# Kernel optimization log

Measured on AMD Instinct MI355X. Metric: run time of the kernel, lower is better.

The kernel has to match this reference:

```python
import jax, jax.numpy as jnp
import numpy as np
import math

B, D, NH, NS, NT = 16, 256, 512, 8, 32
NV = NS * NT          # 256 prediction variables
L, H, A = 4, 8, 64    # attention layers, heads, head dim
HA = H * A            # 512
M = 512               # mlp_dim
R = 128               # resolution
EPS = 1e-5


def setup_inputs() -> dict:
    key = jax.random.key(0)
    ks = jax.random.split(key, 32)
    s = 0.02
    inp = {
        'hist_encoded': jax.random.normal(ks[0], (B, NH, D), jnp.float32),
        'hist_true_u': jax.random.uniform(ks[1], (B, NH), jnp.float32),
        'pred_encoded': jax.random.normal(ks[2], (B, NV, D), jnp.float32),
        'pred_true_u': jax.random.uniform(ks[3], (B, NV), jnp.float32),
        # dimension shifting layer
        'ds_w': jax.random.normal(ks[4], (D, HA), jnp.float32) * s,
        'ds_b': jnp.zeros((HA,), jnp.float32),
        # per-layer, per-head key/value creators: Linear(D+1 -> A)
        'key_w': jax.random.normal(ks[5], (L, H, D + 1, A), jnp.float32) * s,
        'key_b': jnp.zeros((L, H, A), jnp.float32),
        'val_w': jax.random.normal(ks[6], (L, H, D + 1, A), jnp.float32) * s,
        'val_b': jnp.zeros((L, H, A), jnp.float32),
        # layer norms
        'ln1_g': jnp.ones((L, HA), jnp.float32),
        'ln1_b': jnp.zeros((L, HA), jnp.float32),
        'ln2_g': jnp.ones((L, HA), jnp.float32),
        'ln2_b': jnp.zeros((L, HA), jnp.float32),
        # feed-forward (mlp_layers=2): HA->M, M->M, M->HA
        'ff_w1': jax.random.normal(ks[7], (L, HA, M), jnp.float32) * s,
        'ff_b1': jnp.zeros((L, M), jnp.float32),
        'ff_w2': jax.random.normal(ks[8], (L, M, M), jnp.float32) * s,
        'ff_b2': jnp.zeros((L, M), jnp.float32),
        'ff_w3': jax.random.normal(ks[9], (L, M, HA), jnp.float32) * s,
        'ff_b3': jnp.zeros((L, HA), jnp.float32),
        # dist extractor
        'de_w': jax.random.normal(ks[10], (HA, R), jnp.float32) * s,
        'de_b': jnp.zeros((R,), jnp.float32),
        'num_series': NS,
        'num_timesteps': NT,
    }
    return inp


def _ln(x, g, b):
    m = x.mean(-1, keepdims=True)
    v = ((x - m) ** 2).mean(-1, keepdims=True)
    return g * (x - m) / jnp.sqrt(v + EPS) + b


def _forward(hist_encoded, hist_true_u, pred_encoded, pred_true_u,
             ds_w, ds_b, key_w, key_b, val_w, val_b,
             ln1_g, ln1_b, ln2_g, ln2_b,
             ff_w1, ff_b1, ff_w2, ff_b2, ff_w3, ff_b3,
             de_w, de_b):
    Bm, NVm, Dm = pred_encoded.shape
    NHm = hist_encoded.shape[1]
    Lm, Hm, _, Am = key_w.shape
    W = NHm + NVm
    # identity permutation in the source loss() -> no-op
    att = pred_encoded @ ds_w + ds_b  # [B, NV, HA]
    # key/value inputs: [hist||u ; pred||u] -> [B, W, D+1]
    ki = jnp.concatenate([
        jnp.concatenate([hist_encoded, hist_true_u[:, :, None]], axis=2),
        jnp.concatenate([pred_encoded, pred_true_u[:, :, None]], axis=2)], axis=1)
    keys = jnp.einsum('bwd,lhda->lbhwa', ki, key_w) + key_b[:, None, :, None, :]
    vals = jnp.einsum('bwd,lhda->lbhwa', ki, val_w) + val_b[:, None, :, None, :]
    # flipped-triangular mask: position w is masked iff w >= NH + v
    mask = jnp.arange(W)[None, :] >= (NHm + jnp.arange(NVm)[:, None])  # [NV, W]
    scale = Am ** (-0.5)
    for l in range(Lm):
        avh = att.reshape(Bm, NVm, Hm, Am)
        prod = jnp.einsum('bvhi,bhwi->bhvw', avh, keys[l])  # [B,H,NV,W]
        prod = jnp.where(mask, -jnp.inf, prod) * scale
        w = jax.nn.softmax(prod, axis=-1)
        a = jnp.einsum('bhvw,bhwj->bvhj', w, vals[l]).reshape(Bm, NVm, Hm * Am)
        att = _ln(att + a, ln1_g[l], ln1_b[l])
        ff = jnp.maximum(att @ ff_w1[l] + ff_b1[l], 0.0)
        ff = jnp.maximum(ff @ ff_w2[l] + ff_b2[l], 0.0)
        ff = ff @ ff_w3[l] + ff_b3[l]
        att = _ln(att + ff, ln2_g[l], ln2_b[l])
    res = de_w.shape[-1]
    target = jnp.clip(jnp.floor(pred_true_u[:, 1:] * res).astype(jnp.int32), 0, res - 1)
    logits = (att @ de_w + de_b)[:, 1:, :]
    lp = math.log(res) + jax.nn.log_softmax(logits, axis=2)
    lp = jnp.take_along_axis(lp, target[:, :, None], axis=2)[:, :, 0]
    return -lp.sum(axis=1)  # [B]


def reference(hist_encoded, hist_true_u, pred_encoded, pred_true_u,
              ds_w, ds_b, key_w, key_b, val_w, val_b,
              ln1_g, ln1_b, ln2_g, ln2_b,
              ff_w1, ff_b1, ff_w2, ff_b2, ff_w3, ff_b3,
              de_w, de_b, num_series, num_timesteps):
    assert pred_encoded.shape[1] == num_series * num_timesteps
    return _forward(hist_encoded, hist_true_u, pred_encoded, pred_true_u,
                    ds_w, ds_b, key_w, key_b, val_w, val_b,
                    ln1_g, ln1_b, ln2_g, ln2_b,
                    ff_w1, ff_b1, ff_w2, ff_b2, ff_w3, ff_b3,
                    de_w, de_b)
```

## Files before the change

### kernel.cpp

```cpp
#include <hip/hip_runtime.h>

constexpr int kB = 16, kD = 256, kNH = 512, kNV = 256, kW = 768;
constexpr int kL = 4, kH = 8, kA = 64, kHA = 512, kM = 512, kR = 128;
constexpr int kKP = 288;
constexpr int kRows = kB * kNV;

typedef __bf16 bf16x8 __attribute__((ext_vector_type(8)));
typedef __bf16 bf16x4 __attribute__((ext_vector_type(4)));
typedef float f32x4 __attribute__((ext_vector_type(4)));

__device__ inline void load_lds16(const __bf16* g, __bf16* l) {
  __builtin_amdgcn_global_load_lds(
      (const __attribute__((address_space(1))) void*)g,
      (__attribute__((address_space(3))) void*)l, 16, 0, 0);
}

constexpr int kP1 = kB * kW * kKP;
constexpr int kP2 = 4096 * kKP;
constexpr int kP3 = 12 * 512 * 512;
constexpr int kP4 = 200704;
constexpr int kP5 = 16;
constexpr int kPT = kP1 + kP2 + kP3 + kP4 + kP5;

__global__ void prep_kernel(const float* __restrict__ hist,
                            const float* __restrict__ hist_u,
                            const float* __restrict__ pred,
                            const float* __restrict__ pred_u,
                            const float* __restrict__ kw,
                            const float* __restrict__ vw,
                            const float* __restrict__ w1,
                            const float* __restrict__ w2,
                            const float* __restrict__ w3,
                            const float* __restrict__ ds_w,
                            const float* __restrict__ de_w,
                            const float* __restrict__ key_b,
                            const float* __restrict__ val_b,
                            __bf16* __restrict__ ki,
                            __bf16* __restrict__ kvwt,
                            __bf16* __restrict__ ffwt,
                            __bf16* __restrict__ ds_wt,
                            __bf16* __restrict__ de_wt,
                            float* __restrict__ kvb,
                            float* __restrict__ outz) {
  int i = blockIdx.x * 256 + threadIdx.x;
  if (i < kP1) {
    int d = i % kKP;
    int bw = i / kKP;
    int w = bw % kW;
    int b = bw / kW;
    float v = 0.f;
    if (d < 257) {
      if (w < kNH)
        v = (d < kD) ? hist[((size_t)b * kNH + w) * kD + d] : hist_u[b * kNH + w];
      else {
        int p = w - kNH;
        v = (d < kD) ? pred[((size_t)b * kNV + p) * kD + d] : pred_u[b * kNV + p];
      }
    }
    ki[i] = (__bf16)v;
  } else if (i < kP1 + kP2) {
    int j = i - kP1;
    int d = j % kKP;
    int c = j / kKP;
    float v = 0.f;
    if (d < 257) {
      bool isv = c >= 2048;
      int cc = isv ? c - 2048 : c;
      int l = cc >> 9, rest = cc & 511;
      int h = rest >> 6, a = rest & 63;
      size_t src = (((size_t)l * kH + h) * 257 + d) * kA + a;
      v = isv ? vw[src] : kw[src];
    }
    kvwt[j] = (__bf16)v;
  } else if (i < kP1 + kP2 + kP3) {
    int j = i - kP1 - kP2;
    int k = j & 511;
    int n = (j >> 9) & 511;
    int mat = j >> 18;
    int l = mat / 3, which = mat % 3;
    const float* src = which == 0 ? w1 : which == 1 ? w2 : w3;
    ffwt[j] = (__bf16)src[((size_t)l * 512 + k) * 512 + n];
  } else if (i < kP1 + kP2 + kP3 + kP4) {
    int j = i - kP1 - kP2 - kP3;
    if (j < 131072) {
      int n = j >> 8, k = j & 255;
      ds_wt[j] = (__bf16)ds_w[k * 512 + n];
    } else if (j < 196608) {
      int jj = j - 131072;
      int n = jj >> 9, k = jj & 511;
      de_wt[jj] = (__bf16)de_w[k * 128 + n];
    } else {
      int c = j - 196608;
      bool isv = c >= 2048;
      int cc = isv ? c - 2048 : c;
      int l = cc >> 9, rest = cc & 511;
      kvb[c] = isv ? val_b[l * 512 + rest] : key_b[l * 512 + rest];
    }
  } else if (i < kPT) {
    outz[i - kP1 - kP2 - kP3 - kP4] = 0.f;
  }
}

template <int BN, int OMODE, bool RELU, bool KIMAP, bool BIASROW>
__device__ __forceinline__ void gemm_core(
    int bxv, int byv, const __bf16* __restrict__ A,
    const __bf16* __restrict__ Bt, const float* __restrict__ bias,
    void* __restrict__ Cout, __bf16* __restrict__ Cout2, int K, int lda,
    int ldc, __bf16* As, __bf16* Bs) {
  constexpr int JN = BN / 32;
  constexpr int BROWS = BN / 4;
  const int t = threadIdx.x;
  const int wid = t >> 6;
  const int lane = t & 63;
  const int bm = byv * 128;
  const int bn = bxv * BN;
  const int wm = (wid >> 1) * 64;
  const int wn = (wid & 1) * (BN / 2);
  const int sr = lane >> 2, sc = lane & 3;
  const int skey = (sr >> 1) & 3;
  const int abase = KIMAP ? ((bm >> 8) * 768 + 512 + (bm & 255)) : bm;
  const __bf16* Ag = A + (size_t)(abase + wid * 32 + sr) * lda + (sc ^ skey) * 8;
  const __bf16* Bg = Bt + (size_t)(bn + wid * BROWS + sr) * K + (sc ^ skey) * 8;
  __bf16* AsW = As + (wid * 32) * 32;
  __bf16* BsW = Bs + (wid * BROWS) * 32;

  f32x4 acc[4][JN] = {};
  const int q = lane >> 4, mr = lane & 15;
  const int rkey = (mr >> 1) & 3;
  for (int k0 = 0; k0 < K; k0 += 32) {
    if (k0) __syncthreads();
    load_lds16(Ag + k0, AsW);
    load_lds16(Ag + (size_t)16 * lda + k0, AsW + 16 * 32);
    load_lds16(Bg + k0, BsW);
    if (BN == 128) load_lds16(Bg + (size_t)16 * K + k0, BsW + 16 * 32);
    __syncthreads();
    bf16x8 af[4], bfr[JN];
#pragma unroll
    for (int i = 0; i < 4; ++i)
      af[i] = *(const bf16x8*)(As + (wm + i * 16 + mr) * 32 + (q ^ rkey) * 8);
#pragma unroll
    for (int j = 0; j < JN; ++j)
      bfr[j] = *(const bf16x8*)(Bs + (wn + j * 16 + mr) * 32 + (q ^ rkey) * 8);
#pragma unroll
    for (int i = 0; i < 4; ++i)
#pragma unroll
      for (int j = 0; j < JN; ++j)
        acc[i][j] = __builtin_amdgcn_mfma_f32_16x16x32_bf16(af[i], bfr[j],
                                                            acc[i][j], 0, 0, 0);
  }
#pragma unroll
  for (int j = 0; j < JN; ++j) {
    int col = bn + wn + j * 16 + mr;
    float bscol = BIASROW ? 0.f : bias[col];
#pragma unroll
    for (int i = 0; i < 4; ++i) {
      int row0 = bm + wm + i * 16 + q * 4;
#pragma unroll
      for (int r = 0; r < 4; ++r) {
        float v = acc[i][j][r] + (BIASROW ? bias[row0 + r] : bscol);
        if (RELU) v = fmaxf(v, 0.f);
        size_t idx = (size_t)(row0 + r) * ldc + col;
        if (OMODE == 0) {
          ((float*)Cout)[idx] = v;
        } else if (OMODE == 1) {
          ((__bf16*)Cout)[idx] = (__bf16)v;
        } else {
          ((float*)Cout)[idx] = v;
          Cout2[idx] = (__bf16)v;
        }
      }
    }
  }
}

__global__ __launch_bounds__(256) void gemm3_kernel(
    const __bf16* __restrict__ ki, const __bf16* __restrict__ ds_wt,
    const float* __restrict__ ds_b, float* __restrict__ att,
    __bf16* __restrict__ att_bf, const __bf16* __restrict__ kv_wt,
    const float* __restrict__ kvb, __bf16* __restrict__ kvs_k,
    __bf16* __restrict__ vT) {
  __shared__ __align__(16) __bf16 smem[8192];
  __bf16* As = smem;
  __bf16* Bs = smem + 4096;
  int bid = blockIdx.x;
  if (bid < 256) {
    gemm_core<64, 2, false, true, false>(bid & 7, bid >> 3, ki, ds_wt, ds_b,
                                         att, att_bf, 256, kKP, 512, As, Bs);
  } else if (bid < 1792) {
    int b2 = bid - 256;
    gemm_core<128, 1, false, false, false>(b2 & 15, b2 >> 4, ki, kv_wt, kvb,
                                           kvs_k, nullptr, kKP, kKP, 2048, As,
                                           Bs);
  } else {
    int b3 = bid - 1792;
    gemm_core<128, 1, false, false, true>(b3 % 96, b3 / 96,
                                          kv_wt + (size_t)2048 * kKP, ki,
                                          kvb + 2048, vT, nullptr, kKP, kKP,
                                          12288, As, Bs);
  }
}

__global__ __launch_bounds__(256) void attn_kernel(
    const __bf16* __restrict__ attbf, const __bf16* __restrict__ kvs_k,
    const __bf16* __restrict__ vT, __bf16* __restrict__ outbf, int l) {
  const int u = blockIdx.x;
  const int qt = u & 3, h = (u >> 2) & 7, b = u >> 5;
  __shared__ __align__(16) __bf16 Ks[2][64 * 72];
  __shared__ __align__(16) __bf16 Vt[2][64 * 72];
  __shared__ __align__(16) __bf16 Ps[64 * 72];
  const int t = threadIdx.x;
  const int w = t >> 6, lane = t & 63;
  const int quad = lane >> 4, mr = lane & 15;
  bf16x8 aq[2];
  {
    const __bf16* qp = attbf + ((size_t)(b * kNV + qt * 64 + w * 16 + mr) * kHA +
                                h * kA + quad * 8);
    aq[0] = *(const bf16x8*)qp;
    aq[1] = *(const bf16x8*)(qp + 32);
  }
  f32x4 o[4] = {};
  float l_ = 0.f;
  const int cmax = kNH + qt * 64;
  const int pr = t >> 2, pc = t & 3;
  const __bf16* kbase = kvs_k + ((size_t)(b * kW + pr) * 2048 + l * 512 + h * kA);
  const __bf16* vbase = vT + (size_t)(l * 512 + h * kA + pr) * 12288 + b * kW;
  {
    bf16x8 k0 = *(const bf16x8*)(kbase + pc * 8);
    bf16x8 k1 = *(const bf16x8*)(kbase + pc * 8 + 32);
    bf16x8 v0 = *(const bf16x8*)(vbase + pc * 16);
    bf16x8 v1 = *(const bf16x8*)(vbase + pc * 16 + 8);
    *(bf16x8*)&Ks[0][pr * 72 + pc * 8] = k0;
    *(bf16x8*)&Ks[0][pr * 72 + pc * 8 + 32] = k1;
    *(bf16x8*)&Vt[0][pr * 72 + pc * 16] = v0;
    *(bf16x8*)&Vt[0][pr * 72 + pc * 16 + 8] = v1;
  }
  __syncthreads();
  for (int c0 = 0; c0 <= cmax; c0 += 64) {
    const int cur = (c0 >> 6) & 1;
    const bool havenext = (c0 + 64 <= cmax);
    bf16x8 kc0, kc1, vc0, vc1;
    if (havenext) {
      const __bf16* kp = kbase + (size_t)(c0 + 64) * 2048;
      const __bf16* vp = vbase + c0 + 64;
      kc0 = *(const bf16x8*)(kp + pc * 8);
      kc1 = *(const bf16x8*)(kp + pc * 8 + 32);
      vc0 = *(const bf16x8*)(vp + pc * 16);
      vc1 = *(const bf16x8*)(vp + pc * 16 + 8);
    }
    f32x4 s[4];
#pragma unroll
    for (int j = 0; j < 4; ++j) {
      bf16x8 ak0 = *(const bf16x8*)&Ks[cur][(j * 16 + mr) * 72 + quad * 8];
      bf16x8 ak1 = *(const bf16x8*)&Ks[cur][(j * 16 + mr) * 72 + quad * 8 + 32];
      f32x4 z = {};
      z = __builtin_amdgcn_mfma_f32_16x16x32_bf16(ak0, aq[0], z, 0, 0, 0);
      z = __builtin_amdgcn_mfma_f32_16x16x32_bf16(ak1, aq[1], z, 0, 0, 0);
      s[j] = z;
    }
    const int lim = cmax - c0;
    float ev[16];
    float rs = 0.f;
    if (lim >= 64) {
#pragma unroll
      for (int j = 0; j < 4; ++j)
#pragma unroll
        for (int r = 0; r < 4; ++r) {
          float e = __expf(s[j][r] * 0.125f);
          ev[j * 4 + r] = e;
          rs += e;
        }
    } else {
      const int limw = lim + w * 16 + mr;
#pragma unroll
      for (int j = 0; j < 4; ++j)
#pragma unroll
        for (int r = 0; r < 4; ++r) {
          int p = j * 16 + quad * 4 + r;
          float e = (p < limw) ? __expf(s[j][r] * 0.125f) : 0.f;
          ev[j * 4 + r] = e;
          rs += e;
        }
    }
    rs += __shfl_xor(rs, 16);
    rs += __shfl_xor(rs, 32);
    l_ += rs;
#pragma unroll
    for (int j = 0; j < 4; ++j) {
      bf16x4 pk = {(__bf16)ev[j * 4 + 0], (__bf16)ev[j * 4 + 1],
                   (__bf16)ev[j * 4 + 2], (__bf16)ev[j * 4 + 3]};
      *(bf16x4*)&Ps[(w * 16 + mr) * 72 + j * 16 + quad * 4] = pk;
    }
    bf16x8 ap0 = *(const bf16x8*)&Ps[(w * 16 + mr) * 72 + quad * 8];
    bf16x8 ap1 = *(const bf16x8*)&Ps[(w * 16 + mr) * 72 + quad * 8 + 32];
#pragma unroll
    for (int j = 0; j < 4; ++j) {
      bf16x8 b0 = *(const bf16x8*)&Vt[cur][(j * 16 + mr) * 72 + quad * 8];
      bf16x8 b1 = *(const bf16x8*)&Vt[cur][(j * 16 + mr) * 72 + quad * 8 + 32];
      o[j] = __builtin_amdgcn_mfma_f32_16x16x32_bf16(ap0, b0, o[j], 0, 0, 0);
      o[j] = __builtin_amdgcn_mfma_f32_16x16x32_bf16(ap1, b1, o[j], 0, 0, 0);
    }
    if (havenext) {
      *(bf16x8*)&Ks[cur ^ 1][pr * 72 + pc * 8] = kc0;
      *(bf16x8*)&Ks[cur ^ 1][pr * 72 + pc * 8 + 32] = kc1;
      *(bf16x8*)&Vt[cur ^ 1][pr * 72 + pc * 16] = vc0;
      *(bf16x8*)&Vt[cur ^ 1][pr * 72 + pc * 16 + 8] = vc1;
      __syncthreads();
    }
  }
  float invl = 1.f / l_;
#pragma unroll
  for (int r = 0; r < 4; ++r) {
    float ir = __shfl(invl, quad * 4 + r);
    int row = b * kNV + qt * 64 + w * 16 + quad * 4 + r;
#pragma unroll
    for (int j = 0; j < 4; ++j)
      outbf[(size_t)row * kHA + h * kA + j * 16 + mr] = (__bf16)(o[j][r] * ir);
  }
}

__global__ __launch_bounds__(256) void ln_kernel(
    float* __restrict__ att, const __bf16* __restrict__ addbf,
    const float* __restrict__ g, const float* __restrict__ be,
    __bf16* __restrict__ attbf) {
  const int t = threadIdx.x;
  const int wid = t >> 6, lane = t & 63;
#pragma unroll
  for (int i = 0; i < 2; ++i) {
    int row = blockIdx.x * 8 + wid * 2 + i;
    float* ar = att + (size_t)row * kHA + lane * 8;
    float4 x0 = *(float4*)ar;
    float4 x1 = *(float4*)(ar + 4);
    bf16x8 d = *(const bf16x8*)(addbf + (size_t)row * kHA + lane * 8);
    float xs[8] = {x0.x + (float)d[0], x0.y + (float)d[1], x0.z + (float)d[2],
                   x0.w + (float)d[3], x1.x + (float)d[4], x1.y + (float)d[5],
                   x1.z + (float)d[6], x1.w + (float)d[7]};
    float s = 0.f, sq = 0.f;
#pragma unroll
    for (int e = 0; e < 8; ++e) {
      s += xs[e];
      sq += xs[e] * xs[e];
    }
    for (int o = 32; o; o >>= 1) {
      s += __shfl_xor(s, o);
      sq += __shfl_xor(sq, o);
    }
    float mean = s * (1.f / kHA);
    float inv = rsqrtf(sq * (1.f / kHA) - mean * mean + 1e-5f);
    const float* gp = g + lane * 8;
    const float* bp = be + lane * 8;
    float4 g0 = *(const float4*)gp, g1 = *(const float4*)(gp + 4);
    float4 b0 = *(const float4*)bp, b1 = *(const float4*)(bp + 4);
    float ga[8] = {g0.x, g0.y, g0.z, g0.w, g1.x, g1.y, g1.z, g1.w};
    float ba[8] = {b0.x, b0.y, b0.z, b0.w, b1.x, b1.y, b1.z, b1.w};
    float ys[8];
    bf16x8 yb;
#pragma unroll
    for (int e = 0; e < 8; ++e) {
      ys[e] = ga[e] * (xs[e] - mean) * inv + ba[e];
      yb[e] = (__bf16)ys[e];
    }
    *(float4*)ar = make_float4(ys[0], ys[1], ys[2], ys[3]);
    *(float4*)(ar + 4) = make_float4(ys[4], ys[5], ys[6], ys[7]);
    *(bf16x8*)(attbf + (size_t)row * kHA + lane * 8) = yb;
  }
}

template <bool RELU>
__global__ __launch_bounds__(256) void gemm_ff_kernel(
    const __bf16* __restrict__ A, const __bf16* __restrict__ Bt,
    const float* __restrict__ bias, __bf16* __restrict__ Cout) {
  __shared__ __align__(16) __bf16 smem[6144];
  gemm_core<64, 1, RELU, false, false>(blockIdx.x & 7, blockIdx.x >> 3, A, Bt,
                                       bias, Cout, nullptr, 512, 512, 512, smem,
                                       smem + 4096);
}

__global__ __launch_bounds__(256) void de_loss_kernel(
    const __bf16* __restrict__ attbf, const __bf16* __restrict__ de_wt,
    const float* __restrict__ de_b, const float* __restrict__ pred_u,
    float* __restrict__ out) {
  const int blk = blockIdx.x;
  const int t = threadIdx.x;
  const int w = t >> 6, lane = t & 63, quad = lane >> 4, mr = lane & 15;
  const int row0 = blk * 64 + w * 16;
  f32x4 acc[8] = {};
  const __bf16* Ap = attbf + (size_t)(row0 + mr) * kHA + quad * 8;
#pragma unroll 4
  for (int k0 = 0; k0 < 512; k0 += 32) {
    bf16x8 a = *(const bf16x8*)(Ap + k0);
#pragma unroll
    for (int j = 0; j < 8; ++j) {
      bf16x8 bb =
          *(const bf16x8*)(de_wt + (size_t)(j * 16 + mr) * 512 + k0 + quad * 8);
      acc[j] = __builtin_amdgcn_mfma_f32_16x16x32_bf16(a, bb, acc[j], 0, 0, 0);
    }
  }
  float dbv[8];
#pragma unroll
  for (int j = 0; j < 8; ++j) dbv[j] = de_b[j * 16 + mr];
  float lpacc = 0.f;
#pragma unroll
  for (int r = 0; r < 4; ++r) {
    int row = row0 + quad * 4 + r;
    int v = row & 255;
    float lg[8], mx = -1e30f;
#pragma unroll
    for (int j = 0; j < 8; ++j) {
      lg[j] = acc[j][r] + dbv[j];
      mx = fmaxf(mx, lg[j]);
    }
    mx = fmaxf(mx, __shfl_xor(mx, 1));
    mx = fmaxf(mx, __shfl_xor(mx, 2));
    mx = fmaxf(mx, __shfl_xor(mx, 4));
    mx = fmaxf(mx, __shfl_xor(mx, 8));
    float se = 0.f;
#pragma unroll
    for (int j = 0; j < 8; ++j) se += __expf(lg[j] - mx);
    se += __shfl_xor(se, 1);
    se += __shfl_xor(se, 2);
    se += __shfl_xor(se, 4);
    se += __shfl_xor(se, 8);
    float lse = mx + __logf(se);
    float u = pred_u[(row >> 8) * 256 + v];
    int tgt = (int)floorf(u * 128.f);
    tgt = max(0, min(127, tgt));
    float cand = (mr == (tgt & 15)) ? lg[tgt >> 4] : 0.f;
    cand += __shfl_xor(cand, 1);
    cand += __shfl_xor(cand, 2);
    cand += __shfl_xor(cand, 4);
    cand += __shfl_xor(cand, 8);
    float lp = (v >= 1) ? (4.8520302639196171f + cand - lse) : 0.f;
    lpacc += lp;
  }
  lpacc += __shfl_xor(lpacc, 16);
  lpacc += __shfl_xor(lpacc, 32);
  __shared__ float red[4];
  if (lane == 0) red[w] = lpacc;
  __syncthreads();
  if (t == 0)
    atomicAdd(&out[blk >> 2], -(red[0] + red[1] + red[2] + red[3]));
}

extern "C" void kernel_launch(void* const* d_in, const int* in_sizes, int n_in,
                              void* d_out, int out_size, void* d_ws, size_t ws_size,
                              hipStream_t stream) {
  const float* hist   = (const float*)d_in[0];
  const float* hist_u = (const float*)d_in[1];
  const float* pred   = (const float*)d_in[2];
  const float* pred_u = (const float*)d_in[3];
  const float* ds_w   = (const float*)d_in[4];
  const float* ds_b   = (const float*)d_in[5];
  const float* key_w  = (const float*)d_in[6];
  const float* key_b  = (const float*)d_in[7];
  const float* val_w  = (const float*)d_in[8];
  const float* val_b  = (const float*)d_in[9];
  const float* ln1_g  = (const float*)d_in[10];
  const float* ln1_b  = (const float*)d_in[11];
  const float* ln2_g  = (const float*)d_in[12];
  const float* ln2_b  = (const float*)d_in[13];
  const float* ff_w1  = (const float*)d_in[14];
  const float* ff_b1  = (const float*)d_in[15];
  const float* ff_w2  = (const float*)d_in[16];
  const float* ff_b2  = (const float*)d_in[17];
  const float* ff_w3  = (const float*)d_in[18];
  const float* ff_b3  = (const float*)d_in[19];
  const float* de_w   = (const float*)d_in[20];
  const float* de_b   = (const float*)d_in[21];
  float* out = (float*)d_out;

  char* ws = (char*)d_ws;
  size_t off = 0;
  auto alloc = [&](size_t bytes) { char* p = ws + off; off += bytes; return p; };
  __bf16* ki_bf  = (__bf16*)alloc((size_t)kB * kW * kKP * 2);
  __bf16* kv_wt  = (__bf16*)alloc((size_t)4096 * kKP * 2);
  __bf16* ffw_t  = (__bf16*)alloc((size_t)12 * 512 * 512 * 2);
  __bf16* ds_wt  = (__bf16*)alloc((size_t)512 * 256 * 2);
  __bf16* de_wt  = (__bf16*)alloc((size_t)128 * 512 * 2);
  float*  kvb    = (float*)alloc((size_t)4096 * 4);
  __bf16* kvs_k  = (__bf16*)alloc((size_t)kB * kW * 2048 * 2);
  __bf16* vT     = (__bf16*)alloc((size_t)2048 * 12288 * 2);
  float*  att    = (float*)alloc((size_t)kRows * kHA * 4);
  __bf16* att_bf = (__bf16*)alloc((size_t)kRows * kHA * 2);
  __bf16* tmp_bf = (__bf16*)alloc((size_t)kRows * kHA * 2);
  __bf16* ff1_bf = (__bf16*)alloc((size_t)kRows * kM * 2);
  __bf16* ff2_bf = (__bf16*)alloc((size_t)kRows * kM * 2);

  prep_kernel<<<(kPT + 255) / 256, 256, 0, stream>>>(
      hist, hist_u, pred, pred_u, key_w, val_w, ff_w1, ff_w2, ff_w3, ds_w, de_w,
      key_b, val_b, ki_bf, kv_wt, ffw_t, ds_wt, de_wt, kvb, out);

  gemm3_kernel<<<3328, 256, 0, stream>>>(ki_bf, ds_wt, ds_b, att, att_bf, kv_wt,
                                         kvb, kvs_k, vT);

  for (int l = 0; l < kL; ++l) {
    attn_kernel<<<512, 256, 0, stream>>>(att_bf, kvs_k, vT, tmp_bf, l);
    ln_kernel<<<512, 256, 0, stream>>>(att, tmp_bf, ln1_g + l * kHA,
                                       ln1_b + l * kHA, att_bf);
    gemm_ff_kernel<true><<<256, 256, 0, stream>>>(
        att_bf, ffw_t + (size_t)(l * 3) * 262144, ff_b1 + l * kM, ff1_bf);
    gemm_ff_kernel<true><<<256, 256, 0, stream>>>(
        ff1_bf, ffw_t + (size_t)(l * 3 + 1) * 262144, ff_b2 + l * kM, ff2_bf);
    gemm_ff_kernel<false><<<256, 256, 0, stream>>>(
        ff2_bf, ffw_t + (size_t)(l * 3 + 2) * 262144, ff_b3 + l * kHA, tmp_bf);
    ln_kernel<<<512, 256, 0, stream>>>(att, tmp_bf, ln2_g + l * kHA,
                                       ln2_b + l * kHA, att_bf);
  }
  de_loss_kernel<<<64, 256, 0, stream>>>(att_bf, de_wt, de_b, pred_u, out);
}
```

Measured before the change: 475.0 us.

## Fuse layernorms and three-layer feed-forward MLP into one per-layer kernel

```diff
diff --git a/kernel.cpp b/kernel.cpp
--- a/kernel.cpp
+++ b/kernel.cpp
@@ -131,8 +131,9 @@
     if (k0) __syncthreads();
     load_lds16(Ag + k0, AsW);
     load_lds16(Ag + (size_t)16 * lda + k0, AsW + 16 * 32);
-    load_lds16(Bg + k0, BsW);
-    if (BN == 128) load_lds16(Bg + (size_t)16 * K + k0, BsW + 16 * 32);
+#pragma unroll
+    for (int jj = 0; jj < BROWS / 16; ++jj)
+      load_lds16(Bg + (size_t)(jj * 16) * K + k0, BsW + jj * 16 * 32);
     __syncthreads();
     bf16x8 af[4], bfr[JN];
 #pragma unroll
@@ -318,22 +319,35 @@
   }
 }
 
-__global__ __launch_bounds__(256) void ln_kernel(
-    float* __restrict__ att, const __bf16* __restrict__ addbf,
-    const float* __restrict__ g, const float* __restrict__ be,
-    __bf16* __restrict__ attbf) {
+constexpr int kSresLd = 516;
+constexpr int kAbLd = 520;
+
+__global__ __launch_bounds__(256) void ffln_kernel(
+    float* __restrict__ att, const __bf16* __restrict__ tmp_bf,
+    __bf16* __restrict__ att_bf, const __bf16* __restrict__ Wl,
+    const float* __restrict__ fb1, const float* __restrict__ fb2,
+    const float* __restrict__ fb3, const float* __restrict__ g1,
+    const float* __restrict__ bb1, const float* __restrict__ g2,
+    const float* __restrict__ bb2) {
+  __shared__ float Sres[16 * kSresLd];
+  __shared__ __bf16 Ab[16 * kAbLd];
+  __shared__ __bf16 Cb[16 * kAbLd];
   const int t = threadIdx.x;
-  const int wid = t >> 6, lane = t & 63;
-#pragma unroll
-  for (int i = 0; i < 2; ++i) {
-    int row = blockIdx.x * 8 + wid * 2 + i;
-    float* ar = att + (size_t)row * kHA + lane * 8;
-    float4 x0 = *(float4*)ar;
-    float4 x1 = *(float4*)(ar + 4);
-    bf16x8 d = *(const bf16x8*)(addbf + (size_t)row * kHA + lane * 8);
-    float xs[8] = {x0.x + (float)d[0], x0.y + (float)d[1], x0.z + (float)d[2],
-                   x0.w + (float)d[3], x1.x + (float)d[4], x1.y + (float)d[5],
-                   x1.z + (float)d[6], x1.w + (float)d[7]};
+  const int w = t >> 6, lane = t & 63;
+  const int quad = lane >> 4, mr = lane & 15;
+  const int blk = blockIdx.x;
+#pragma unroll
+  for (int r = 0; r < 4; ++r) {
+    const int rl = w * 4 + r;
+    const int row = blk * 16 + rl;
+    const float* ap = att + (size_t)row * 512 + lane * 8;
+    float4 a0 = *(const float4*)ap;
+    float4 a1 = *(const float4*)(ap + 4);
+    bf16x8 tv = *(const bf16x8*)(tmp_bf + (size_t)row * 512 + lane * 8);
+    float xs[8] = {a0.x + (float)tv[0], a0.y + (float)tv[1],
+                   a0.z + (float)tv[2], a0.w + (float)tv[3],
+                   a1.x + (float)tv[4], a1.y + (float)tv[5],
+                   a1.z + (float)tv[6], a1.w + (float)tv[7]};
     float s = 0.f, sq = 0.f;
 #pragma unroll
     for (int e = 0; e < 8; ++e) {
@@ -346,12 +360,12 @@
     }
     float mean = s * (1.f / kHA);
     float inv = rsqrtf(sq * (1.f / kHA) - mean * mean + 1e-5f);
-    const float* gp = g + lane * 8;
-    const float* bp = be + lane * 8;
-    float4 g0 = *(const float4*)gp, g1 = *(const float4*)(gp + 4);
-    float4 b0 = *(const float4*)bp, b1 = *(const float4*)(bp + 4);
-    float ga[8] = {g0.x, g0.y, g0.z, g0.w, g1.x, g1.y, g1.z, g1.w};
-    float ba[8] = {b0.x, b0.y, b0.z, b0.w, b1.x, b1.y, b1.z, b1.w};
+    float4 gv0 = *(const float4*)(g1 + lane * 8);
+    float4 gv1 = *(const float4*)(g1 + lane * 8 + 4);
+    float4 bv0 = *(const float4*)(bb1 + lane * 8);
+    float4 bv1 = *(const float4*)(bb1 + lane * 8 + 4);
+    float ga[8] = {gv0.x, gv0.y, gv0.z, gv0.w, gv1.x, gv1.y, gv1.z, gv1.w};
+    float ba[8] = {bv0.x, bv0.y, bv0.z, bv0.w, bv1.x, bv1.y, bv1.z, bv1.w};
     float ys[8];
     bf16x8 yb;
 #pragma unroll
@@ -359,20 +373,116 @@
       ys[e] = ga[e] * (xs[e] - mean) * inv + ba[e];
       yb[e] = (__bf16)ys[e];
     }
-    *(float4*)ar = make_float4(ys[0], ys[1], ys[2], ys[3]);
-    *(float4*)(ar + 4) = make_float4(ys[4], ys[5], ys[6], ys[7]);
-    *(bf16x8*)(attbf + (size_t)row * kHA + lane * 8) = yb;
-  }
-}
-
-template <bool RELU>
-__global__ __launch_bounds__(256) void gemm_ff_kernel(
-    const __bf16* __restrict__ A, const __bf16* __restrict__ Bt,
-    const float* __restrict__ bias, __bf16* __restrict__ Cout) {
-  __shared__ __align__(16) __bf16 smem[6144];
-  gemm_core<64, 1, RELU, false, false>(blockIdx.x & 7, blockIdx.x >> 3, A, Bt,
-                                       bias, Cout, nullptr, 512, 512, 512, smem,
-                                       smem + 4096);
+    *(float4*)&Sres[rl * kSresLd + lane * 8] =
+        make_float4(ys[0], ys[1], ys[2], ys[3]);
+    *(float4*)&Sres[rl * kSresLd + lane * 8 + 4] =
+        make_float4(ys[4], ys[5], ys[6], ys[7]);
+    *(bf16x8*)&Ab[rl * kAbLd + lane * 8] = yb;
+  }
+  __syncthreads();
+  const int wn = w * 128;
+  {
+    f32x4 acc[8] = {};
+    const __bf16* Wp = Wl + (size_t)(wn + mr) * 512 + quad * 8;
+    for (int k0 = 0; k0 < 512; k0 += 32) {
+      bf16x8 af = *(const bf16x8*)&Ab[mr * kAbLd + k0 + quad * 8];
+#pragma unroll
+      for (int j = 0; j < 8; ++j) {
+        bf16x8 bfv = *(const bf16x8*)(Wp + (size_t)j * 16 * 512 + k0);
+        acc[j] = __builtin_amdgcn_mfma_f32_16x16x32_bf16(af, bfv, acc[j], 0, 0, 0);
+      }
+    }
+#pragma unroll
+    for (int j = 0; j < 8; ++j) {
+      int col = wn + j * 16 + mr;
+      float bs = fb1[col];
+#pragma unroll
+      for (int r = 0; r < 4; ++r)
+        Cb[(quad * 4 + r) * kAbLd + col] = (__bf16)fmaxf(acc[j][r] + bs, 0.f);
+    }
+  }
+  __syncthreads();
+  {
+    f32x4 acc[8] = {};
+    const __bf16* Wp = Wl + 262144 + (size_t)(wn + mr) * 512 + quad * 8;
+    for (int k0 = 0; k0 < 512; k0 += 32) {
+      bf16x8 af = *(const bf16x8*)&Cb[mr * kAbLd + k0 + quad * 8];
+#pragma unroll
+      for (int j = 0; j < 8; ++j) {
+        bf16x8 bfv = *(const bf16x8*)(Wp + (size_t)j * 16 * 512 + k0);
+        acc[j] = __builtin_amdgcn_mfma_f32_16x16x32_bf16(af, bfv, acc[j], 0, 0, 0);
+      }
+    }
+#pragma unroll
+    for (int j = 0; j < 8; ++j) {
+      int col = wn + j * 16 + mr;
+      float bs = fb2[col];
+#pragma unroll
+      for (int r = 0; r < 4; ++r)
+        Ab[(quad * 4 + r) * kAbLd + col] = (__bf16)fmaxf(acc[j][r] + bs, 0.f);
+    }
+  }
+  __syncthreads();
+  {
+    f32x4 acc[8] = {};
+    const __bf16* Wp = Wl + 524288 + (size_t)(wn + mr) * 512 + quad * 8;
+    for (int k0 = 0; k0 < 512; k0 += 32) {
+      bf16x8 af = *(const bf16x8*)&Ab[mr * kAbLd + k0 + quad * 8];
+#pragma unroll
+      for (int j = 0; j < 8; ++j) {
+        bf16x8 bfv = *(const bf16x8*)(Wp + (size_t)j * 16 * 512 + k0);
+        acc[j] = __builtin_amdgcn_mfma_f32_16x16x32_bf16(af, bfv, acc[j], 0, 0, 0);
+      }
+    }
+#pragma unroll
+    for (int j = 0; j < 8; ++j) {
+      int col = wn + j * 16 + mr;
+      float bs = fb3[col];
+#pragma unroll
+      for (int r = 0; r < 4; ++r) {
+        float* sp = &Sres[(quad * 4 + r) * kSresLd + col];
+        *sp = *sp + acc[j][r] + bs;
+      }
+    }
+  }
+  __syncthreads();
+#pragma unroll
+  for (int r = 0; r < 4; ++r) {
+    const int rl = w * 4 + r;
+    const int row = blk * 16 + rl;
+    float4 x0 = *(const float4*)&Sres[rl * kSresLd + lane * 8];
+    float4 x1 = *(const float4*)&Sres[rl * kSresLd + lane * 8 + 4];
+    float xs[8] = {x0.x, x0.y, x0.z, x0.w, x1.x, x1.y, x1.z, x1.w};
+    float s = 0.f, sq = 0.f;
+#pragma unroll
+    for (int e = 0; e < 8; ++e) {
+      s += xs[e];
+      sq += xs[e] * xs[e];
+    }
+    for (int o = 32; o; o >>= 1) {
+      s += __shfl_xor(s, o);
+      sq += __shfl_xor(sq, o);
+    }
+    float mean = s * (1.f / kHA);
+    float inv = rsqrtf(sq * (1.f / kHA) - mean * mean + 1e-5f);
+    float4 gv0 = *(const float4*)(g2 + lane * 8);
+    float4 gv1 = *(const float4*)(g2 + lane * 8 + 4);
+    float4 bv0 = *(const float4*)(bb2 + lane * 8);
+    float4 bv1 = *(const float4*)(bb2 + lane * 8 + 4);
+    float ga[8] = {gv0.x, gv0.y, gv0.z, gv0.w, gv1.x, gv1.y, gv1.z, gv1.w};
+    float ba[8] = {bv0.x, bv0.y, bv0.z, bv0.w, bv1.x, bv1.y, bv1.z, bv1.w};
+    float ys[8];
+    bf16x8 yb;
+#pragma unroll
+    for (int e = 0; e < 8; ++e) {
+      ys[e] = ga[e] * (xs[e] - mean) * inv + ba[e];
+      yb[e] = (__bf16)ys[e];
+    }
+    float* op = att + (size_t)row * 512 + lane * 8;
+    *(float4*)op = make_float4(ys[0], ys[1], ys[2], ys[3]);
+    *(float4*)(op + 4) = make_float4(ys[4], ys[5], ys[6], ys[7]);
+    *(bf16x8*)(att_bf + (size_t)row * 512 + lane * 8) = yb;
+  }
 }
 
 __global__ __launch_bounds__(256) void de_loss_kernel(
@@ -482,8 +592,6 @@
   float*  att    = (float*)alloc((size_t)kRows * kHA * 4);
   __bf16* att_bf = (__bf16*)alloc((size_t)kRows * kHA * 2);
   __bf16* tmp_bf = (__bf16*)alloc((size_t)kRows * kHA * 2);
-  __bf16* ff1_bf = (__bf16*)alloc((size_t)kRows * kM * 2);
-  __bf16* ff2_bf = (__bf16*)alloc((size_t)kRows * kM * 2);
 
   prep_kernel<<<(kPT + 255) / 256, 256, 0, stream>>>(
       hist, hist_u, pred, pred_u, key_w, val_w, ff_w1, ff_w2, ff_w3, ds_w, de_w,
@@ -494,16 +602,10 @@
 
   for (int l = 0; l < kL; ++l) {
     attn_kernel<<<512, 256, 0, stream>>>(att_bf, kvs_k, vT, tmp_bf, l);
-    ln_kernel<<<512, 256, 0, stream>>>(att, tmp_bf, ln1_g + l * kHA,
-                                       ln1_b + l * kHA, att_bf);
-    gemm_ff_kernel<true><<<256, 256, 0, stream>>>(
-        att_bf, ffw_t + (size_t)(l * 3) * 262144, ff_b1 + l * kM, ff1_bf);
-    gemm_ff_kernel<true><<<256, 256, 0, stream>>>(
-        ff1_bf, ffw_t + (size_t)(l * 3 + 1) * 262144, ff_b2 + l * kM, ff2_bf);
-    gemm_ff_kernel<false><<<256, 256, 0, stream>>>(
-        ff2_bf, ffw_t + (size_t)(l * 3 + 2) * 262144, ff_b3 + l * kHA, tmp_bf);
-    ln_kernel<<<512, 256, 0, stream>>>(att, tmp_bf, ln2_g + l * kHA,
-                                       ln2_b + l * kHA, att_bf);
+    ffln_kernel<<<256, 256, 0, stream>>>(
+        att, tmp_bf, att_bf, ffw_t + (size_t)(l * 3) * 262144, ff_b1 + l * kM,
+        ff_b2 + l * kM, ff_b3 + l * kHA, ln1_g + l * kHA, ln1_b + l * kHA,
+        ln2_g + l * kHA, ln2_b + l * kHA);
   }
   de_loss_kernel<<<64, 256, 0, stream>>>(att_bf, de_wt, de_b, pred_u, out);
 }
```

After: 503.9 us. +6.1%, slower.
